# Optimization experiments

Measured on AMD Instinct MI355X. Metric: run time of the kernel, lower is better.

Reference implementation:

```python
import jax, jax.numpy as jnp
import numpy as np

N_NODES = 100000
N_EDGES = 1000000
D_IN = 64
D_MODEL = 64  # H * D
H = 4
D = D_MODEL // H


def setup_inputs() -> dict:
    key = jax.random.key(0)
    ks = jax.random.split(key, 9)
    nodes = jax.random.normal(ks[0], (N_NODES, D_IN), dtype=jnp.float32)
    senders = jax.random.randint(ks[1], (N_EDGES,), 0, N_NODES, dtype=jnp.int32)
    receivers = jnp.sort(jax.random.randint(ks[2], (N_EDGES,), 0, N_NODES, dtype=jnp.int32))
    s = 1.0 / np.sqrt(D_IN)
    W_qk = jax.random.uniform(ks[3], (D_IN, D_MODEL), jnp.float32, -s, s)
    b_qk = jnp.zeros((D_MODEL,), jnp.float32)
    W_v = jax.random.uniform(ks[4], (D_IN, D_MODEL), jnp.float32, -s, s)
    b_v = jnp.zeros((D_MODEL,), jnp.float32)
    so = 1.0 / np.sqrt(D_MODEL)
    W_out = jax.random.uniform(ks[5], (D_MODEL, D_MODEL), jnp.float32, -so, so)
    b_out = jnp.zeros((D_MODEL,), jnp.float32)
    return {
        'nodes': nodes, 'W_qk': W_qk, 'b_qk': b_qk, 'W_v': W_v, 'b_v': b_v,
        'W_out': W_out, 'b_out': b_out, 'senders': senders, 'receivers': receivers,
    }


def _segment_softmax(logits, segment_ids, num_segments):
    # jraph-style numerically stable segment softmax (segments are sorted)
    maxs = jax.ops.segment_max(logits, segment_ids, num_segments, indices_are_sorted=True)
    e = jnp.exp(logits - maxs[segment_ids])
    z = jax.ops.segment_sum(e, segment_ids, num_segments, indices_are_sorted=True)
    return e / z[segment_ids]


def reference(nodes, W_qk, b_qk, W_v, b_v, W_out, b_out, senders, receivers):
    N = nodes.shape[0]
    # projections: N (H D) -> N H D
    qks = (nodes @ W_qk + b_qk).reshape(N, H, D)
    vs = (nodes @ W_v + b_v).reshape(N, H, D)
    # per-edge QK scores: [E, H]
    scores = jnp.einsum('ehd,ehd->eh', qks[receivers], qks[senders])
    attn = _segment_softmax(scores, receivers, N)
    # weighted message scatter: [E,H,D] -> [N, H*D]
    messages = (attn[..., None] * vs[senders]).reshape(-1, H * D)
    ctx = jax.ops.segment_sum(messages, receivers, N, indices_are_sorted=True)
    out = ctx @ W_out + b_out
    return out, attn
```

## Files before the change

kernel.cpp:

```cpp
#include <hip/hip_runtime.h>
#include <math.h>


typedef _Float16 h2 __attribute__((ext_vector_type(2)));
typedef _Float16 half8 __attribute__((ext_vector_type(8)));
typedef float floatx4 __attribute__((ext_vector_type(4)));

#define SP_ROW 136

__global__ __launch_bounds__(256) void mhga_prep(
    const float* __restrict__ Wqk, const float* __restrict__ Wv,
    _Float16* __restrict__ Wt,
    const int* __restrict__ receivers, int* __restrict__ row_ptr,
    int N, int E)
{
    if ((int)blockIdx.x < 32) {
        const int idx = blockIdx.x * 256 + threadIdx.x;
        const int n = idx >> 6, k = idx & 63;
        const float w = (n < 64) ? Wqk[k * 64 + n] : Wv[k * 64 + (n - 64)];
        Wt[idx] = (_Float16)w;
        return;
    }
    const int n = (blockIdx.x - 32) * 256 + threadIdx.x;
    if (n > N) return;
    int lo = 0, hi = E;
    while (lo < hi) {
        const int mid = (lo + hi) >> 1;
        if (receivers[mid] < n) lo = mid + 1; else hi = mid;
    }
    row_ptr[n] = lo;
}

__global__ __launch_bounds__(256) void mhga_proj(
    const float* __restrict__ X, const _Float16* __restrict__ Wt,
    const float* __restrict__ bqk, const float* __restrict__ bv,
    unsigned char* __restrict__ packed, int N)
{
    __shared__ __align__(16) _Float16 sP[64 * SP_ROW];
    const int t = threadIdx.x;
    const int w = t >> 6, lane = t & 63;
    const int ln = lane & 15, quad = lane >> 4;
    const int m0 = blockIdx.x * 64;

    const int arow = min(m0 + w * 16 + ln, N - 1);
    const float* xr = X + (size_t)arow * 64;
    const float4 xa = *(const float4*)(xr + quad * 8);
    const float4 xb = *(const float4*)(xr + quad * 8 + 4);
    const float4 xc = *(const float4*)(xr + 32 + quad * 8);
    const float4 xd = *(const float4*)(xr + 32 + quad * 8 + 4);
    const half8 a0 = { (_Float16)xa.x, (_Float16)xa.y, (_Float16)xa.z,
                       (_Float16)xa.w, (_Float16)xb.x, (_Float16)xb.y,
                       (_Float16)xb.z, (_Float16)xb.w };
    const half8 a1 = { (_Float16)xc.x, (_Float16)xc.y, (_Float16)xc.z,
                       (_Float16)xc.w, (_Float16)xd.x, (_Float16)xd.y,
                       (_Float16)xd.z, (_Float16)xd.w };

    floatx4 acc[8];
#pragma unroll
    for (int tt = 0; tt < 8; ++tt) {
        const _Float16* wrow = Wt + (tt * 16 + ln) * 64;
        const half8 b0 = *(const half8*)(wrow + quad * 8);
        const half8 b1 = *(const half8*)(wrow + 32 + quad * 8);
        floatx4 c = {0.f, 0.f, 0.f, 0.f};
        c = __builtin_amdgcn_mfma_f32_16x16x32_f16(a0, b0, c, 0, 0, 0);
        c = __builtin_amdgcn_mfma_f32_16x16x32_f16(a1, b1, c, 0, 0, 0);
        acc[tt] = c;
    }

#pragma unroll
    for (int tt = 0; tt < 8; ++tt) {
        const float bt = (tt < 4) ? bqk[tt * 16 + ln] : bv[(tt - 4) * 16 + ln];
        const int j = (tt & 3) * 16 + ln;
        const int fidx = (j >> 2) * 8 + ((tt < 4) ? 0 : 4) + (j & 3);
#pragma unroll
        for (int r = 0; r < 4; ++r) {
            const int lrow = w * 16 + quad * 4 + r;
            sP[lrow * SP_ROW + fidx] = (_Float16)(acc[tt][r] + bt);
        }
    }

    const int crow = w * 16 + (lane >> 2);
    const int grow = m0 + crow;
    if (grow < N) {
        const _Float16* src = sP + crow * SP_ROW + (lane & 3) * 32;
        unsigned char* dst = packed + (size_t)grow * 256 + (lane & 3) * 64;
#pragma unroll
        for (int c = 0; c < 4; ++c)
            *(uint4*)(dst + c * 16) = *(const uint4*)(src + c * 8);
    }
}

__global__ __launch_bounds__(256) void mhga_attn(
    const unsigned char* __restrict__ packed,
    const int* __restrict__ senders, const int* __restrict__ row_ptr,
    const float* __restrict__ Wout, const float* __restrict__ bout,
    float* __restrict__ out, float* __restrict__ attn_out, int N)
{
    __shared__ float sW[64 * 64];
    __shared__ float sCtx[4][64];
    __shared__ float sAtt[4][256];
    const int t = threadIdx.x;
#pragma unroll
    for (int i = t * 4; i < 4096; i += 1024)
        *(float4*)(sW + i) = *(const float4*)(Wout + i);

    const int wave = t >> 6, lane = t & 63;
    const int g = lane >> 4, tl = lane & 15;
    const float bo = bout[lane];
    __syncthreads();

    for (int n = blockIdx.x * 4 + wave; n < N; n += gridDim.x * 4) {
        const int e0 = row_ptr[n];
        const int e1 = row_ptr[n + 1];
        const int cnt = e1 - e0;

        float l = 0.f;
        float4 ctx = make_float4(0.f, 0.f, 0.f, 0.f);
        const uint4 qpk = *(const uint4*)(packed + (size_t)n * 256 + tl * 16);
        const h2 q0 = __builtin_bit_cast(h2, qpk.x);
        const h2 q1 = __builtin_bit_cast(h2, qpk.y);

        if (cnt <= 64) {
            int sid = 0;
            if (e0 + lane < e1) sid = senders[e0 + lane];
            const int iters = (cnt + 3) >> 2;
            const int s0 = __shfl(sid, g, 64);
            uint4 pk = *(const uint4*)(packed + (size_t)s0 * 256 + tl * 16);
            for (int i = 0; i < iters; ++i) {
                uint4 pkn = pk;
                if (i + 1 < iters) {
                    const int sn = __shfl(sid, (i + 1) * 4 + g, 64);
                    pkn = *(const uint4*)(packed + (size_t)sn * 256 + tl * 16);
                }
                const int idx = i * 4 + g;
                const h2 k0 = __builtin_bit_cast(h2, pk.x);
                const h2 k1 = __builtin_bit_cast(h2, pk.y);
                const h2 v0 = __builtin_bit_cast(h2, pk.z);
                const h2 v1 = __builtin_bit_cast(h2, pk.w);
                float d = __builtin_amdgcn_fdot2(q0, k0, 0.f, false);
                d = __builtin_amdgcn_fdot2(q1, k1, d, false);
                d += __shfl_xor(d, 1, 64);
                d += __shfl_xor(d, 2, 64);
                float p = __expf(d);
                p = (idx < cnt) ? p : 0.f;
                if ((tl & 3) == 0)
                    sAtt[wave][idx * 4 + (tl >> 2)] = p;
                l += p;
                ctx.x = fmaf(p, (float)v0.x, ctx.x);
                ctx.y = fmaf(p, (float)v0.y, ctx.y);
                ctx.z = fmaf(p, (float)v1.x, ctx.z);
                ctx.w = fmaf(p, (float)v1.y, ctx.w);
                pk = pkn;
            }
        } else {
            for (int base = e0; base < e1; base += 64) {
                const int c2 = min(64, e1 - base);
                int sid2 = 0;
                if (base + lane < e1) sid2 = senders[base + lane];
                const int it2 = (c2 + 3) >> 2;
                for (int i = 0; i < it2; ++i) {
                    const int idx = i * 4 + g;
                    const int s = __shfl(sid2, idx, 64);
                    if (idx < c2) {
                        const uint4 pk =
                            *(const uint4*)(packed + (size_t)s * 256 + tl * 16);
                        const h2 k0 = __builtin_bit_cast(h2, pk.x);
                        const h2 k1 = __builtin_bit_cast(h2, pk.y);
                        const h2 v0 = __builtin_bit_cast(h2, pk.z);
                        const h2 v1 = __builtin_bit_cast(h2, pk.w);
                        float d = __builtin_amdgcn_fdot2(q0, k0, 0.f, false);
                        d = __builtin_amdgcn_fdot2(q1, k1, d, false);
                        d += __shfl_xor(d, 1, 64);
                        d += __shfl_xor(d, 2, 64);
                        const float p = __expf(d);
                        if ((tl & 3) == 0)
                            attn_out[(size_t)(base + idx) * 4 + (tl >> 2)] = p;
                        l += p;
                        ctx.x = fmaf(p, (float)v0.x, ctx.x);
                        ctx.y = fmaf(p, (float)v0.y, ctx.y);
                        ctx.z = fmaf(p, (float)v1.x, ctx.z);
                        ctx.w = fmaf(p, (float)v1.y, ctx.w);
                    }
                }
            }
        }

#pragma unroll
        for (int mask = 16; mask <= 32; mask <<= 1) {
            l     += __shfl_xor(l, mask, 64);
            ctx.x += __shfl_xor(ctx.x, mask, 64);
            ctx.y += __shfl_xor(ctx.y, mask, 64);
            ctx.z += __shfl_xor(ctx.z, mask, 64);
            ctx.w += __shfl_xor(ctx.w, mask, 64);
        }
        const float inv = (l > 0.f) ? (1.f / l) : 0.f;
        if (g == 0) {
            *(float4*)(&sCtx[wave][tl * 4]) =
                make_float4(ctx.x * inv, ctx.y * inv, ctx.z * inv, ctx.w * inv);
        }

        const float lh = __shfl(l, (lane & 3) << 2, 64);
        const float invl = (lh > 0.f) ? (1.f / lh) : 0.f;
        if (cnt <= 64) {
            const int cnt4 = cnt * 4;
            for (int f = lane; f < cnt4; f += 64)
                attn_out[e0 * 4 + f] = sAtt[wave][f] * invl;
        } else {
            __builtin_amdgcn_s_waitcnt(0x0F70);
            volatile const float* vp = attn_out;
            for (int f = e0 * 4 + lane; f < e1 * 4; f += 64)
                attn_out[f] = vp[f] * invl;
        }

        float acc = bo;
#pragma unroll
        for (int k = 0; k < 64; k += 4) {
            const float4 c = *(const float4*)(&sCtx[wave][k]);
            acc = fmaf(c.x, sW[(k + 0) * 64 + lane], acc);
            acc = fmaf(c.y, sW[(k + 1) * 64 + lane], acc);
            acc = fmaf(c.z, sW[(k + 2) * 64 + lane], acc);
            acc = fmaf(c.w, sW[(k + 3) * 64 + lane], acc);
        }
        out[(size_t)n * 64 + lane] = acc;
    }
}

extern "C" void kernel_launch(void* const* d_in, const int* in_sizes, int n_in,
                              void* d_out, int out_size, void* d_ws, size_t ws_size,
                              hipStream_t stream) {
    const float* nodes   = (const float*)d_in[0];
    const float* W_qk    = (const float*)d_in[1];
    const float* b_qk    = (const float*)d_in[2];
    const float* W_v     = (const float*)d_in[3];
    const float* b_v     = (const float*)d_in[4];
    const float* W_out   = (const float*)d_in[5];
    const float* b_out   = (const float*)d_in[6];
    const int* senders   = (const int*)d_in[7];
    const int* receivers = (const int*)d_in[8];

    const int N = in_sizes[0] / 64;
    const int E = in_sizes[7];

    float* out      = (float*)d_out;
    float* attn_out = out + (size_t)N * 64;

    unsigned char* packed = (unsigned char*)d_ws;
    int*   rowp = (int*)(packed + (size_t)N * 256);
    float* spare = (float*)(rowp + (((N + 1) + 3) & ~3));
    _Float16* Wt = (_Float16*)(spare + (size_t)E * 4);

    const int RB = (N + 1 + 255) / 256;
    mhga_prep<<<32 + RB, 256, 0, stream>>>(W_qk, W_v, Wt, receivers, rowp, N, E);
    mhga_proj<<<(N + 63) / 64, 256, 0, stream>>>(nodes, Wt, b_qk, b_v,
                                                 packed, N);
    mhga_attn<<<1792, 256, 0, stream>>>(packed, senders, rowp,
                                        W_out, b_out, out, attn_out, N);
}
```

Before: 192.2 us.

## Split output projection into separate MFMA kernel with fp16 context buffer

Moves the per-node W_out matmul out of the attention kernel, which previously did scalar FMAs against a 16KB LDS copy of W_out per wave. The attention kernel now writes the normalized context as fp16 to a workspace buffer, and a new kernel applies W_out using 16x16x32 f16 MFMA. W_out is transposed to fp16 in the prep kernel alongside the other weights, and the attention grid grows from 1792 to 2048 blocks. This frees LDS and the sync in the attention kernel, likely raising occupancy. The cost is an extra launch, an fp16 round trip of the context through global memory, and reduced precision in the output projection.

```diff
diff --git a/kernel.cpp b/kernel.cpp
--- a/kernel.cpp
+++ b/kernel.cpp
@@ -10,18 +10,20 @@
 
 __global__ __launch_bounds__(256) void mhga_prep(
     const float* __restrict__ Wqk, const float* __restrict__ Wv,
-    _Float16* __restrict__ Wt,
+    const float* __restrict__ Wout, _Float16* __restrict__ Wt,
     const int* __restrict__ receivers, int* __restrict__ row_ptr,
     int N, int E)
 {
-    if ((int)blockIdx.x < 32) {
+    if ((int)blockIdx.x < 48) {
         const int idx = blockIdx.x * 256 + threadIdx.x;
         const int n = idx >> 6, k = idx & 63;
-        const float w = (n < 64) ? Wqk[k * 64 + n] : Wv[k * 64 + (n - 64)];
+        const float w = (n < 64) ? Wqk[k * 64 + n]
+                      : (n < 128) ? Wv[k * 64 + (n - 64)]
+                      : Wout[k * 64 + (n - 128)];
         Wt[idx] = (_Float16)w;
         return;
     }
-    const int n = (blockIdx.x - 32) * 256 + threadIdx.x;
+    const int n = (blockIdx.x - 48) * 256 + threadIdx.x;
     if (n > N) return;
     int lo = 0, hi = E;
     while (lo < hi) {
@@ -93,21 +95,12 @@
 __global__ __launch_bounds__(256) void mhga_attn(
     const unsigned char* __restrict__ packed,
     const int* __restrict__ senders, const int* __restrict__ row_ptr,
-    const float* __restrict__ Wout, const float* __restrict__ bout,
-    float* __restrict__ out, float* __restrict__ attn_out, int N)
-{
-    __shared__ float sW[64 * 64];
-    __shared__ float sCtx[4][64];
+    _Float16* __restrict__ ctxb, float* __restrict__ attn_out, int N)
+{
     __shared__ float sAtt[4][256];
     const int t = threadIdx.x;
-#pragma unroll
-    for (int i = t * 4; i < 4096; i += 1024)
-        *(float4*)(sW + i) = *(const float4*)(Wout + i);
-
     const int wave = t >> 6, lane = t & 63;
     const int g = lane >> 4, tl = lane & 15;
-    const float bo = bout[lane];
-    __syncthreads();
 
     for (int n = blockIdx.x * 4 + wave; n < N; n += gridDim.x * 4) {
         const int e0 = row_ptr[n];
@@ -194,10 +187,6 @@
             ctx.w += __shfl_xor(ctx.w, mask, 64);
         }
         const float inv = (l > 0.f) ? (1.f / l) : 0.f;
-        if (g == 0) {
-            *(float4*)(&sCtx[wave][tl * 4]) =
-                make_float4(ctx.x * inv, ctx.y * inv, ctx.z * inv, ctx.w * inv);
-        }
 
         const float lh = __shfl(l, (lane & 3) << 2, 64);
         const float invl = (lh > 0.f) ? (1.f / lh) : 0.f;
@@ -212,16 +201,52 @@
                 attn_out[f] = vp[f] * invl;
         }
 
-        float acc = bo;
-#pragma unroll
-        for (int k = 0; k < 64; k += 4) {
-            const float4 c = *(const float4*)(&sCtx[wave][k]);
-            acc = fmaf(c.x, sW[(k + 0) * 64 + lane], acc);
-            acc = fmaf(c.y, sW[(k + 1) * 64 + lane], acc);
-            acc = fmaf(c.z, sW[(k + 2) * 64 + lane], acc);
-            acc = fmaf(c.w, sW[(k + 3) * 64 + lane], acc);
-        }
-        out[(size_t)n * 64 + lane] = acc;
+        if (g == 0) {
+            const h2 c01 = { (_Float16)(ctx.x * inv), (_Float16)(ctx.y * inv) };
+            const h2 c23 = { (_Float16)(ctx.z * inv), (_Float16)(ctx.w * inv) };
+            uint2 pc;
+            pc.x = __builtin_bit_cast(unsigned int, c01);
+            pc.y = __builtin_bit_cast(unsigned int, c23);
+            *(uint2*)(ctxb + (size_t)n * 64 + tl * 4) = pc;
+        }
+    }
+}
+
+__global__ __launch_bounds__(256) void mhga_out(
+    const _Float16* __restrict__ ctxb, const _Float16* __restrict__ Wt,
+    const float* __restrict__ bout, float* __restrict__ out, int N)
+{
+    const int t = threadIdx.x;
+    const int w = t >> 6, lane = t & 63;
+    const int ln = lane & 15, quad = lane >> 4;
+    const int m0 = blockIdx.x * 64;
+
+    const int arow = min(m0 + w * 16 + ln, N - 1);
+    const _Float16* ar = ctxb + (size_t)arow * 64;
+    const half8 a0 = *(const half8*)(ar + quad * 8);
+    const half8 a1 = *(const half8*)(ar + 32 + quad * 8);
+
+    floatx4 acc[4];
+#pragma unroll
+    for (int tt = 0; tt < 4; ++tt) {
+        const _Float16* wrow = Wt + (size_t)(128 + tt * 16 + ln) * 64;
+        const half8 b0 = *(const half8*)(wrow + quad * 8);
+        const half8 b1 = *(const half8*)(wrow + 32 + quad * 8);
+        floatx4 c = {0.f, 0.f, 0.f, 0.f};
+        c = __builtin_amdgcn_mfma_f32_16x16x32_f16(a0, b0, c, 0, 0, 0);
+        c = __builtin_amdgcn_mfma_f32_16x16x32_f16(a1, b1, c, 0, 0, 0);
+        acc[tt] = c;
+    }
+
+#pragma unroll
+    for (int tt = 0; tt < 4; ++tt) {
+        const float bt = bout[tt * 16 + ln];
+#pragma unroll
+        for (int r = 0; r < 4; ++r) {
+            const int grow = m0 + w * 16 + quad * 4 + r;
+            if (grow < N)
+                out[(size_t)grow * 64 + tt * 16 + ln] = acc[tt][r] + bt;
+        }
     }
 }
 
@@ -247,12 +272,15 @@
     unsigned char* packed = (unsigned char*)d_ws;
     int*   rowp = (int*)(packed + (size_t)N * 256);
     float* spare = (float*)(rowp + (((N + 1) + 3) & ~3));
+    _Float16* ctxb = (_Float16*)spare;
     _Float16* Wt = (_Float16*)(spare + (size_t)E * 4);
 
     const int RB = (N + 1 + 255) / 256;
-    mhga_prep<<<32 + RB, 256, 0, stream>>>(W_qk, W_v, Wt, receivers, rowp, N, E);
+    mhga_prep<<<48 + RB, 256, 0, stream>>>(W_qk, W_v, W_out, Wt,
+                                           receivers, rowp, N, E);
     mhga_proj<<<(N + 63) / 64, 256, 0, stream>>>(nodes, Wt, b_qk, b_v,
                                                  packed, N);
-    mhga_attn<<<1792, 256, 0, stream>>>(packed, senders, rowp,
-                                        W_out, b_out, out, attn_out, N);
-}
+    mhga_attn<<<2048, 256, 0, stream>>>(packed, senders, rowp,
+                                        ctxb, attn_out, N);
+    mhga_out<<<(N + 63) / 64, 256, 0, stream>>>(ctxb, Wt, b_out, out, N);
+}
```

Result: no change. 195.5 us (+1.7%).
